# Performance work log

Hardware: AMD Instinct MI355X
Metric: run time of the kernel (lower is better)

The kernel has to match this reference:

```python
import jax, jax.numpy as jnp
import numpy as np

E = 64          # num_expert
DIN = 512       # d_input
DOUT = 512      # d_output
T = 131072      # total routed tokens (sum of fwd_expert_count)


def setup_inputs() -> dict:
    key = jax.random.key(0)
    k1, k2, k3 = jax.random.split(key, 3)
    inp = jax.random.normal(k1, (T, DIN), dtype=jnp.float32)
    # FMoELinear params: weight [E, d_out, d_in], bias [E, d_out]
    weight = jax.random.normal(k2, (E, DOUT, DIN), dtype=jnp.float32) * (1.0 / np.sqrt(DIN))
    bias = jax.random.normal(k3, (E, DOUT), dtype=jnp.float32) * 0.01
    # Irregular per-expert token counts summing exactly to T (host-side int64,
    # as in fastmoe where fwd_expert_count lives on CPU and drives dispatch).
    rng = np.random.default_rng(0)
    counts = rng.multinomial(T, np.full(E, 1.0 / E))
    fwd_expert_count = np.asarray(counts, dtype=np.int64)
    return {"inp": inp, "weight": weight, "bias": bias, "fwd_expert_count": fwd_expert_count}


def reference(inp, weight, bias, fwd_expert_count):
    # Grouped GEMM: tokens are sorted by expert; expert e owns rows
    # [offs[e], offs[e+1]).  y_i = x_i @ W_e^T + b_e.
    counts = np.asarray(fwd_expert_count)
    offs = np.concatenate([[0], np.cumsum(counts)])
    outs = []
    for e in range(counts.shape[0]):  # fixed small loop over experts
        xe = inp[int(offs[e]):int(offs[e + 1])]          # [n_e, d_in]
        outs.append(xe @ weight[e].T + bias[e])          # [n_e, d_out]
    return jnp.concatenate(outs, axis=0)                 # [T, d_out]
```

## Files before the change

kernel.cpp:

```cpp
#include <hip/hip_runtime.h>
#include <hip/hip_bf16.h>
#include <stdint.h>

#define NE    64
#define DIN   512
#define DOUT  512
#define TTOK  131072
#define BM    128
#define BN    256
#define BK    32
#define NK    (DIN / BK)
#define TILES_TOTAL (TTOK / BM + NE)
#define NXCD  8
#define TPX   (TILES_TOTAL / NXCD)

typedef __bf16 bf16x8_t __attribute__((ext_vector_type(8)));
typedef float  f32x4_t  __attribute__((ext_vector_type(4)));

#define ABUF(i) ((i) * 8192)
#define BBUF(i) (16384 + (i) * 16384)
#define LDS_BYTES 49152

#define WAITV0() asm volatile("s_waitcnt vmcnt(0)" ::: "memory")
#define LGKM0()  asm volatile("s_waitcnt lgkmcnt(0)" ::: "memory")
#define SB() __builtin_amdgcn_sched_barrier(0)

#define WBF_OFF 32768

__global__ void setup_tiles(const int* __restrict__ cnt, int* __restrict__ ws) {
    int e = threadIdx.x;
    if (e >= NE) return;
    int off = 0, tbase = 0;
    for (int i = 0; i < e; ++i) {
        int c = cnt[i];
        off += c;
        tbase += (c + (BM - 1)) / BM;
    }
    int c = cnt[e];
    int nt = (c + (BM - 1)) / BM;
    int* tbl = ws + 4;
    for (int t = 0; t < nt; ++t) {
        int idx = tbase + t;
        tbl[4 * idx + 0] = e;
        tbl[4 * idx + 1] = off + t * BM;
        tbl[4 * idx + 2] = off + c;
        tbl[4 * idx + 3] = 0;
    }
    if (e == NE - 1) ws[0] = tbase + nt;
}

__global__ __launch_bounds__(256) void wcvt(const float* __restrict__ w,
                                            __bf16* __restrict__ wbf) {
    const size_t stride = (size_t)gridDim.x * 256;
    size_t i = (size_t)blockIdx.x * 256 + threadIdx.x;
    const size_t n8 = (size_t)NE * DOUT * DIN / 8;
    for (; i < n8; i += stride) {
        f32x4_t a = *(const f32x4_t*)(w + i * 8);
        f32x4_t b = *(const f32x4_t*)(w + i * 8 + 4);
        bf16x8_t h;
#pragma unroll
        for (int j = 0; j < 4; ++j) {
            h[j]     = (__bf16)a[j];
            h[4 + j] = (__bf16)b[j];
        }
        *(bf16x8_t*)(wbf + i * 8) = h;
    }
}

__device__ __forceinline__ void gload16(const void* g, uint8_t* l) {
    __builtin_amdgcn_global_load_lds(
        (const __attribute__((address_space(1))) uint32_t*)g,
        (__attribute__((address_space(3))) uint32_t*)l, 16, 0, 0);
}

__global__ __launch_bounds__(512, 4) void moe_gemm(
    const float* __restrict__ inp,
    const __bf16* __restrict__ wbf,
    const float* __restrict__ bias,
    const int* __restrict__ ws,
    float* __restrict__ out)
{
    __shared__ __align__(16) uint8_t smem[LDS_BYTES];

    const int bid  = blockIdx.x;
    const int xcd  = bid & (NXCD - 1);
    const int slot = bid >> 3;
    const int tile = xcd * TPX + (slot >> 1);
    const int n0   = (slot & 1) * BN;

    const int ntiles = ws[0];
    if (tile >= ntiles) return;
    const int4 ti = ((const int4*)(ws + 4))[tile];
    const int e = ti.x, row0 = ti.y, row_end = ti.z;

    const int tid  = threadIdx.x;
    const int lane = tid & 63;
    const int wave = tid >> 6;
    const int dr = lane >> 3;
    const int ac = lane & 7;
    const int u  = ac ^ dr;

    const __bf16* bsrc[2];
#pragma unroll
    for (int i = 0; i < 2; ++i) {
        int lr = wave * 16 + i * 8 + dr;
        int dout = n0 + lr + ((u >> 2) << 7);
        bsrc[i] = wbf + (size_t)(e * DOUT + dout) * DIN + (u & 3) * 8;
    }
    auto issueB = [&](int t, int buf) {
        uint8_t* dst = smem + BBUF(buf) + wave * 2048;
#pragma unroll
        for (int i = 0; i < 2; ++i)
            gload16(bsrc[i] + t * BK, dst + i * 1024);
    };

    const int alr = tid >> 3;
    const int acn = tid & 7;
    int agrow = row0 + alr + ((acn >> 2) << 6);
    if (agrow > row_end - 1) agrow = row_end - 1;
    const float* asrc = inp + (size_t)agrow * DIN + (acn & 3) * 8;
    const int awoff = alr * 128 + ((acn * 16) ^ ((alr & 7) << 4));

    f32x4_t ra[2];
    auto loadA = [&](int t) {
        ra[0] = *(const f32x4_t*)(asrc + t * BK);
        ra[1] = *(const f32x4_t*)(asrc + t * BK + 4);
    };
    auto writeA = [&](int buf) {
        bf16x8_t h;
#pragma unroll
        for (int j = 0; j < 4; ++j) {
            h[j]     = (__bf16)ra[0][j];
            h[4 + j] = (__bf16)ra[1][j];
        }
        *(bf16x8_t*)(smem + ABUF(buf) + awoff) = h;
    };

    const int wr = (wave >> 2) * 64;
    const int wc = (wave & 3) * 64;
    const int frow = lane & 15;
    const int kg   = lane >> 4;

    f32x4_t acc[4][4] = {};

    auto compute = [&](int buf) {
        bf16x8_t af[4], bg[4];
#pragma unroll
        for (int m = 0; m < 4; ++m) {
            const int row = wr + m * 16 + frow;
            const int lr  = row & 63;
            const int h   = row >> 6;
            af[m] = *(const bf16x8_t*)(smem + ABUF(buf) + lr * 128 +
                                       ((h * 64 + kg * 16) ^ ((lr & 7) << 4)));
        }
#pragma unroll
        for (int n = 0; n < 4; ++n) {
            const int row = wc + n * 16 + frow;
            const int lr  = row & 127;
            const int h   = row >> 7;
            bg[n] = *(const bf16x8_t*)(smem + BBUF(buf) + lr * 128 +
                                       ((h * 64 + kg * 16) ^ ((lr & 7) << 4)));
        }
        __builtin_amdgcn_s_setprio(1);
#pragma unroll
        for (int m = 0; m < 4; ++m)
#pragma unroll
            for (int n = 0; n < 4; ++n)
                acc[m][n] = __builtin_amdgcn_mfma_f32_16x16x32_bf16(
                    af[m], bg[n], acc[m][n], 0, 0, 0);
        __builtin_amdgcn_s_setprio(0);
    };

    loadA(0);
    issueB(0, 0);
    writeA(0);
    WAITV0(); LGKM0(); SB();
    __builtin_amdgcn_s_barrier();
#pragma unroll
    for (int t = 0; t < NK; ++t) {
        const int buf = t & 1;
        if (t + 1 < NK) {
            loadA(t + 1);
            SB();
            issueB(t + 1, buf ^ 1);
            SB();
        }
        compute(buf);
        if (t + 1 < NK) {
            writeA(buf ^ 1);
            WAITV0(); LGKM0(); SB();
            __builtin_amdgcn_s_barrier();
        }
    }

    const int crow = kg * 4;
    const int ccol = frow;
    float bv[4];
#pragma unroll
    for (int n = 0; n < 4; ++n)
        bv[n] = bias[e * DOUT + n0 + wc + n * 16 + ccol];
#pragma unroll
    for (int m = 0; m < 4; ++m) {
#pragma unroll
        for (int j = 0; j < 4; ++j) {
            const int grow = row0 + wr + m * 16 + crow + j;
            if (grow < row_end) {
                float* orow = out + (size_t)grow * DOUT + n0 + wc + ccol;
#pragma unroll
                for (int n = 0; n < 4; ++n)
                    orow[n * 16] = acc[m][n][j] + bv[n];
            }
        }
    }
}

extern "C" void kernel_launch(void* const* d_in, const int* in_sizes, int n_in,
                              void* d_out, int out_size, void* d_ws, size_t ws_size,
                              hipStream_t stream) {
    const float* inp    = (const float*)d_in[0];
    const float* weight = (const float*)d_in[1];
    const float* bias   = (const float*)d_in[2];
    const int* cnt      = (const int*)d_in[3];
    float* out = (float*)d_out;
    int* ws = (int*)d_ws;
    __bf16* wbf = (__bf16*)((char*)d_ws + WBF_OFF);

    hipLaunchKernelGGL(setup_tiles, dim3(1), dim3(64), 0, stream, cnt, ws);
    hipLaunchKernelGGL(wcvt, dim3(2048), dim3(256), 0, stream, weight, wbf);
    hipLaunchKernelGGL(moe_gemm, dim3(TILES_TOTAL * 2), dim3(512), 0, stream,
                       inp, wbf, bias, ws, out);
}
```

Before: 205.8 us.

## Deepen GEMM K-loop prefetch to distance two with triple-buffered B tiles

```diff
diff --git a/kernel.cpp b/kernel.cpp
--- a/kernel.cpp
+++ b/kernel.cpp
@@ -19,9 +19,9 @@
 
 #define ABUF(i) ((i) * 8192)
 #define BBUF(i) (16384 + (i) * 16384)
-#define LDS_BYTES 49152
-
-#define WAITV0() asm volatile("s_waitcnt vmcnt(0)" ::: "memory")
+#define LDS_BYTES 65536
+
+#define WAITV(n) asm volatile("s_waitcnt vmcnt(" #n ")" ::: "memory")
 #define LGKM0()  asm volatile("s_waitcnt lgkmcnt(0)" ::: "memory")
 #define SB() __builtin_amdgcn_sched_barrier(0)
 
@@ -107,8 +107,8 @@
         int dout = n0 + lr + ((u >> 2) << 7);
         bsrc[i] = wbf + (size_t)(e * DOUT + dout) * DIN + (u & 3) * 8;
     }
-    auto issueB = [&](int t, int buf) {
-        uint8_t* dst = smem + BBUF(buf) + wave * 2048;
+    auto issueB = [&](int t, int slot3) {
+        uint8_t* dst = smem + BBUF(slot3) + wave * 2048;
 #pragma unroll
         for (int i = 0; i < 2; ++i)
             gload16(bsrc[i] + t * BK, dst + i * 1024);
@@ -121,19 +121,19 @@
     const float* asrc = inp + (size_t)agrow * DIN + (acn & 3) * 8;
     const int awoff = alr * 128 + ((acn * 16) ^ ((alr & 7) << 4));
 
-    f32x4_t ra[2];
+    f32x4_t ra[2][2];
     auto loadA = [&](int t) {
-        ra[0] = *(const f32x4_t*)(asrc + t * BK);
-        ra[1] = *(const f32x4_t*)(asrc + t * BK + 4);
-    };
-    auto writeA = [&](int buf) {
+        ra[t & 1][0] = *(const f32x4_t*)(asrc + t * BK);
+        ra[t & 1][1] = *(const f32x4_t*)(asrc + t * BK + 4);
+    };
+    auto writeA = [&](int t) {
         bf16x8_t h;
 #pragma unroll
         for (int j = 0; j < 4; ++j) {
-            h[j]     = (__bf16)ra[0][j];
-            h[4 + j] = (__bf16)ra[1][j];
-        }
-        *(bf16x8_t*)(smem + ABUF(buf) + awoff) = h;
+            h[j]     = (__bf16)ra[t & 1][0][j];
+            h[4 + j] = (__bf16)ra[t & 1][1][j];
+        }
+        *(bf16x8_t*)(smem + ABUF(t & 1) + awoff) = h;
     };
 
     const int wr = (wave >> 2) * 64;
@@ -143,14 +143,15 @@
 
     f32x4_t acc[4][4] = {};
 
-    auto compute = [&](int buf) {
+    auto compute = [&](int t) {
+        const int abuf = t & 1, bs = t % 3;
         bf16x8_t af[4], bg[4];
 #pragma unroll
         for (int m = 0; m < 4; ++m) {
             const int row = wr + m * 16 + frow;
             const int lr  = row & 63;
             const int h   = row >> 6;
-            af[m] = *(const bf16x8_t*)(smem + ABUF(buf) + lr * 128 +
+            af[m] = *(const bf16x8_t*)(smem + ABUF(abuf) + lr * 128 +
                                        ((h * 64 + kg * 16) ^ ((lr & 7) << 4)));
         }
 #pragma unroll
@@ -158,7 +159,7 @@
             const int row = wc + n * 16 + frow;
             const int lr  = row & 127;
             const int h   = row >> 7;
-            bg[n] = *(const bf16x8_t*)(smem + BBUF(buf) + lr * 128 +
+            bg[n] = *(const bf16x8_t*)(smem + BBUF(bs) + lr * 128 +
                                        ((h * 64 + kg * 16) ^ ((lr & 7) << 4)));
         }
         __builtin_amdgcn_s_setprio(1);
@@ -171,24 +172,24 @@
         __builtin_amdgcn_s_setprio(0);
     };
 
-    loadA(0);
-    issueB(0, 0);
+    loadA(0); SB();
+    issueB(0, 0); SB();
+    loadA(1); SB();
+    issueB(1, 1); SB();
     writeA(0);
-    WAITV0(); LGKM0(); SB();
+    WAITV(4); LGKM0(); SB();
     __builtin_amdgcn_s_barrier();
 #pragma unroll
     for (int t = 0; t < NK; ++t) {
-        const int buf = t & 1;
+        if (t + 2 < NK) {
+            loadA(t + 2); SB();
+            issueB(t + 2, (t + 2) % 3); SB();
+        }
+        compute(t);
         if (t + 1 < NK) {
-            loadA(t + 1);
-            SB();
-            issueB(t + 1, buf ^ 1);
-            SB();
-        }
-        compute(buf);
-        if (t + 1 < NK) {
-            writeA(buf ^ 1);
-            WAITV0(); LGKM0(); SB();
+            writeA(t + 1);
+            if (t + 2 < NK) { WAITV(4); } else { WAITV(0); }
+            LGKM0(); SB();
             __builtin_amdgcn_s_barrier();
         }
     }
```

After: 210.3 us. 1.02x slower.
